# Kernel optimization log

Hardware: AMD Instinct MI355X
Metric: run time of the kernel (lower is better)

Reference implementation:

```python
import jax, jax.numpy as jnp
import numpy as np

IN_DIM = 128
OUT_DIM = 128
N_NEIGH = 32
BATCH = 8192


def setup_inputs() -> dict:
    key = jax.random.key(0)
    k1, k2, k3, k4, k5 = jax.random.split(key, 5)
    ai_sq = jax.random.normal(k1, (BATCH, IN_DIM), dtype=jnp.float32)
    ai_sn = jax.random.normal(k2, (N_NEIGH, BATCH, IN_DIM), dtype=jnp.float32)
    # nn.Linear params (weight [out,in], bias [out]) and attention vector u [2*out]
    W_w = jax.random.normal(k3, (OUT_DIM, IN_DIM), dtype=jnp.float32) / np.sqrt(IN_DIM)
    W_b = jax.random.normal(k4, (OUT_DIM,), dtype=jnp.float32) * 0.01
    u = jax.random.normal(k5, (2 * OUT_DIM,), dtype=jnp.float32)
    return {"ai_sq": ai_sq, "ai_sn": ai_sn, "W_w": W_w, "W_b": W_b, "u": u}


def reference(ai_sq, ai_sn, W_w, W_b, u):
    out_dim = W_w.shape[0]
    # shared linear projection W
    sq_proj = ai_sq @ W_w.T + W_b                      # [B, D]
    sn_proj = jnp.einsum('nbi,oi->nbo', ai_sn, W_w) + W_b  # [N, B, D]
    # u . concat(sq_proj, sn_proj) == u1.sq_proj + u2.sn_proj
    u1, u2 = u[:out_dim], u[out_dim:]
    mult = (sq_proj @ u1)[None, :] + jnp.einsum('nbd,d->nb', sn_proj, u2)  # [N, B]
    beta = jnp.exp(jax.nn.leaky_relu(mult, negative_slope=0.01))           # [N, B]
    return beta / jnp.sum(beta, axis=0)                # softmax-like normalize over neighbors
```

## Files before the change

kernel.cpp:

```cpp
#include <hip/hip_runtime.h>
#include <math.h>

#define IN_DIM   128
#define OUT_DIM  128
#define N_NEIGH  32
#define BATCH    8192
#define B_TILE   8

__global__ __launch_bounds__(1024) void prep_kernel(const float* __restrict__ W_w,
                                                    const float* __restrict__ W_b,
                                                    const float* __restrict__ u,
                                                    float* __restrict__ ws) {
    const int tid = threadIdx.x;
    const int i = tid & 127;
    const int g = tid >> 7;

    float a1 = 0.f, a2 = 0.f;
    #pragma unroll
    for (int oo = 0; oo < 16; ++oo) {
        int o = g * 16 + oo;
        float w = W_w[o * IN_DIM + i];
        a1 += w * u[o];
        a2 += w * u[OUT_DIM + o];
    }

    __shared__ float r1[8][128];
    __shared__ float r2[8][128];
    r1[g][i] = a1;
    r2[g][i] = a2;

    __shared__ float red[128];
    if (tid < 128) red[tid] = W_b[tid] * (u[tid] + u[OUT_DIM + tid]);
    __syncthreads();

    if (g == 0) {
        float s1 = 0.f, s2 = 0.f;
        #pragma unroll
        for (int gg = 0; gg < 8; ++gg) { s1 += r1[gg][i]; s2 += r2[gg][i]; }
        ws[i] = s1;
        ws[IN_DIM + i] = s2;
    }
    __syncthreads();
    if (tid == 0) {
        float s = 0.f;
        for (int k = 0; k < 128; ++k) s += red[k];
        ws[2 * IN_DIM] = s;
    }
}

__global__ __launch_bounds__(256) void gat_kernel(const float* __restrict__ ai_sq,
                                                  const float* __restrict__ ai_sn,
                                                  const float* __restrict__ ws,
                                                  float* __restrict__ out) {
    const int b0   = blockIdx.x * B_TILE;
    const int tid  = threadIdx.x;
    const int wave = tid >> 6;
    const int lane = tid & 63;
    const int c    = lane & 31;
    const int hb   = lane >> 5;

    __shared__ float t[33][B_TILE + 1];

    const float4* v1 = (const float4*)ws;
    const float4* v2 = (const float4*)(ws + IN_DIM);
    const float   cc = ws[2 * IN_DIM];
    const float4  v1c = v1[c];
    const float4  v2c = v2[c];

    for (int r = wave; r < 33; r += 4) {
        const float* base = (r < 32)
            ? (ai_sn + ((size_t)r * BATCH + b0) * IN_DIM)
            : (ai_sq + (size_t)b0 * IN_DIM);
        const float4 vv = (r < 32) ? v2c : v1c;
        #pragma unroll
        for (int k = 0; k < B_TILE / 2; ++k) {
            const int bl = k * 2 + hb;
            float4 x = ((const float4*)(base + (size_t)bl * IN_DIM))[c];
            float p = x.x * vv.x + x.y * vv.y + x.z * vv.z + x.w * vv.w;
            #pragma unroll
            for (int m = 16; m > 0; m >>= 1) p += __shfl_xor(p, m);
            if (c == 0) t[r][bl] = p;
        }
    }
    __syncthreads();

    const int n  = tid & 31;
    const int bl = tid >> 5;
    float mult = t[n][bl] + t[32][bl] + cc;
    float l = mult > 0.f ? mult : 0.01f * mult;
    float mx = l;
    #pragma unroll
    for (int m = 16; m > 0; m >>= 1) mx = fmaxf(mx, __shfl_xor(mx, m));
    float e = expf(l - mx);
    float s = e;
    #pragma unroll
    for (int m = 16; m > 0; m >>= 1) s += __shfl_xor(s, m);
    float res = e / s;
    __syncthreads();
    t[n][bl] = res;
    __syncthreads();

    const int nn = tid >> 3;
    const int bb = tid & 7;
    out[(size_t)nn * BATCH + b0 + bb] = t[nn][bb];
}

extern "C" void kernel_launch(void* const* d_in, const int* in_sizes, int n_in,
                              void* d_out, int out_size, void* d_ws, size_t ws_size,
                              hipStream_t stream) {
    const float* ai_sq = (const float*)d_in[0];
    const float* ai_sn = (const float*)d_in[1];
    const float* W_w   = (const float*)d_in[2];
    const float* W_b   = (const float*)d_in[3];
    const float* u     = (const float*)d_in[4];
    float* out = (float*)d_out;
    float* ws  = (float*)d_ws;

    prep_kernel<<<1, 1024, 0, stream>>>(W_w, W_b, u, ws);
    gat_kernel<<<BATCH / B_TILE, 256, 0, stream>>>(ai_sq, ai_sn, ws, out);
}
```

Baseline: 203.3 us.

## Fuse weight-vector prep into main kernel and software-pipeline neighbor loads

Removes the separate single-block prep kernel: each block recomputes W^T·u1, W^T·u2 and the bias constant into shared memory, then runs the attention computation. The main loop now has each wave handle one batch row across all 32 neighbors, with register double-buffering of four float4 loads per step and a segmented shuffle reduction that reduces four dot products together. The batch tile doubles to 16 with 512 threads. This removes one launch and the serial dependency on prep, and raises memory-level parallelism. The cost is redundant reads of the 64KB weight matrix in every block (512 blocks), served mostly from cache.

After: 203.4 us. No clear change (+0.1%).

```diff
diff --git a/kernel.cpp b/kernel.cpp
--- a/kernel.cpp
+++ b/kernel.cpp
@@ -5,104 +5,127 @@
 #define OUT_DIM  128
 #define N_NEIGH  32
 #define BATCH    8192
-#define B_TILE   8
+#define B_TILE   16
+#define THREADS  512
 
-__global__ __launch_bounds__(1024) void prep_kernel(const float* __restrict__ W_w,
-                                                    const float* __restrict__ W_b,
-                                                    const float* __restrict__ u,
-                                                    float* __restrict__ ws) {
+__global__ __launch_bounds__(THREADS) void gat_fused(const float* __restrict__ ai_sq,
+                                                     const float* __restrict__ ai_sn,
+                                                     const float* __restrict__ W_w,
+                                                     const float* __restrict__ W_b,
+                                                     const float* __restrict__ u,
+                                                     float* __restrict__ out) {
     const int tid = threadIdx.x;
-    const int i = tid & 127;
-    const int g = tid >> 7;
+    const int b0  = blockIdx.x * B_TILE;
 
-    float a1 = 0.f, a2 = 0.f;
-    #pragma unroll
-    for (int oo = 0; oo < 16; ++oo) {
-        int o = g * 16 + oo;
-        float w = W_w[o * IN_DIM + i];
-        a1 += w * u[o];
-        a2 += w * u[OUT_DIM + o];
+    __shared__ __align__(16) float v1s[IN_DIM];
+    __shared__ __align__(16) float v2s[IN_DIM];
+    __shared__ float r1s[4][IN_DIM];
+    __shared__ float r2s[4][IN_DIM];
+    __shared__ float ccs;
+
+    {
+        const int i = tid & 127;
+        const int g = tid >> 7;
+        float a1 = 0.f, a2 = 0.f;
+        #pragma unroll 8
+        for (int oo = 0; oo < 32; ++oo) {
+            const int o = g * 32 + oo;
+            const float w = W_w[o * IN_DIM + i];
+            a1 = fmaf(w, u[o], a1);
+            a2 = fmaf(w, u[OUT_DIM + o], a2);
+        }
+        r1s[g][i] = a1;
+        r2s[g][i] = a2;
+        if (tid < 64) {
+            float s = W_b[tid]      * (u[tid]      + u[OUT_DIM + tid])
+                    + W_b[tid + 64] * (u[tid + 64] + u[OUT_DIM + tid + 64]);
+            #pragma unroll
+            for (int m = 32; m > 0; m >>= 1) s += __shfl_xor(s, m);
+            if (tid == 0) ccs = s;
+        }
+        __syncthreads();
+        if (tid < 128) {
+            v1s[tid] = r1s[0][tid] + r1s[1][tid] + r1s[2][tid] + r1s[3][tid];
+            v2s[tid] = r2s[0][tid] + r2s[1][tid] + r2s[2][tid] + r2s[3][tid];
+        }
+        __syncthreads();
     }
 
-    __shared__ float r1[8][128];
-    __shared__ float r2[8][128];
-    r1[g][i] = a1;
-    r2[g][i] = a2;
-
-    __shared__ float red[128];
-    if (tid < 128) red[tid] = W_b[tid] * (u[tid] + u[OUT_DIM + tid]);
-    __syncthreads();
-
-    if (g == 0) {
-        float s1 = 0.f, s2 = 0.f;
-        #pragma unroll
-        for (int gg = 0; gg < 8; ++gg) { s1 += r1[gg][i]; s2 += r2[gg][i]; }
-        ws[i] = s1;
-        ws[IN_DIM + i] = s2;
-    }
-    __syncthreads();
-    if (tid == 0) {
-        float s = 0.f;
-        for (int k = 0; k < 128; ++k) s += red[k];
-        ws[2 * IN_DIM] = s;
-    }
-}
-
-__global__ __launch_bounds__(256) void gat_kernel(const float* __restrict__ ai_sq,
-                                                  const float* __restrict__ ai_sn,
-                                                  const float* __restrict__ ws,
-                                                  float* __restrict__ out) {
-    const int b0   = blockIdx.x * B_TILE;
-    const int tid  = threadIdx.x;
-    const int wave = tid >> 6;
     const int lane = tid & 63;
+    const int w    = tid >> 6;
     const int c    = lane & 31;
     const int hb   = lane >> 5;
+    const int bl   = 2 * w + hb;
+    const float4 v1c = ((const float4*)v1s)[c];
+    const float4 v2c = ((const float4*)v2s)[c];
+    const float  cc  = ccs;
 
-    __shared__ float t[33][B_TILE + 1];
+    __shared__ float t[N_NEIGH + 1][B_TILE + 1];
 
-    const float4* v1 = (const float4*)ws;
-    const float4* v2 = (const float4*)(ws + IN_DIM);
-    const float   cc = ws[2 * IN_DIM];
-    const float4  v1c = v1[c];
-    const float4  v2c = v2[c];
+    const size_t RS = (size_t)BATCH * (IN_DIM / 4);
+    const float4* p   = (const float4*)ai_sn + (size_t)(b0 + bl) * (IN_DIM / 4) + c;
+    const float4* psq = (const float4*)ai_sq + (size_t)(b0 + bl) * (IN_DIM / 4) + c;
 
-    for (int r = wave; r < 33; r += 4) {
-        const float* base = (r < 32)
-            ? (ai_sn + ((size_t)r * BATCH + b0) * IN_DIM)
-            : (ai_sq + (size_t)b0 * IN_DIM);
-        const float4 vv = (r < 32) ? v2c : v1c;
+    float4 q0 = p[0], q1 = p[RS], q2 = p[2 * RS], q3 = p[3 * RS];
+    #pragma unroll
+    for (int g = 0; g < 8; ++g) {
+        float4 n0, n1, n2, n3;
+        if (g < 7) {
+            const float4* pn = p + (size_t)(4 * g + 4) * RS;
+            n0 = pn[0]; n1 = pn[RS]; n2 = pn[2 * RS]; n3 = pn[3 * RS];
+        } else {
+            n0 = psq[0]; n1 = n0; n2 = n0; n3 = n0;
+        }
+        float d0 = fmaf(q0.x, v2c.x, fmaf(q0.y, v2c.y, fmaf(q0.z, v2c.z, q0.w * v2c.w)));
+        float d1 = fmaf(q1.x, v2c.x, fmaf(q1.y, v2c.y, fmaf(q1.z, v2c.z, q1.w * v2c.w)));
+        float d2 = fmaf(q2.x, v2c.x, fmaf(q2.y, v2c.y, fmaf(q2.z, v2c.z, q2.w * v2c.w)));
+        float d3 = fmaf(q3.x, v2c.x, fmaf(q3.y, v2c.y, fmaf(q3.z, v2c.z, q3.w * v2c.w)));
+
+        d0 += __shfl_xor(d0, 16); d1 += __shfl_xor(d1, 16);
+        d2 += __shfl_xor(d2, 16); d3 += __shfl_xor(d3, 16);
+        float e01 = (lane & 16) ? d1 : d0;
+        float e23 = (lane & 16) ? d3 : d2;
+        e01 += __shfl_xor(e01, 8);
+        e23 += __shfl_xor(e23, 8);
+        float z = (lane & 8) ? e23 : e01;
+        z += __shfl_xor(z, 4); z += __shfl_xor(z, 2); z += __shfl_xor(z, 1);
+        if ((lane & 7) == 0) {
+            const int rr = 4 * g + ((lane >> 3) & 1) * 2 + ((lane >> 4) & 1);
+            t[rr][bl] = z;
+        }
+        q0 = n0; q1 = n1; q2 = n2; q3 = n3;
+    }
+    {
+        float d = fmaf(q0.x, v1c.x, fmaf(q0.y, v1c.y, fmaf(q0.z, v1c.z, q0.w * v1c.w)));
         #pragma unroll
-        for (int k = 0; k < B_TILE / 2; ++k) {
-            const int bl = k * 2 + hb;
-            float4 x = ((const float4*)(base + (size_t)bl * IN_DIM))[c];
-            float p = x.x * vv.x + x.y * vv.y + x.z * vv.z + x.w * vv.w;
-            #pragma unroll
-            for (int m = 16; m > 0; m >>= 1) p += __shfl_xor(p, m);
-            if (c == 0) t[r][bl] = p;
-        }
+        for (int m = 16; m > 0; m >>= 1) d += __shfl_xor(d, m);
+        if (c == 0) t[N_NEIGH][bl] = d;
     }
     __syncthreads();
 
-    const int n  = tid & 31;
-    const int bl = tid >> 5;
-    float mult = t[n][bl] + t[32][bl] + cc;
-    float l = mult > 0.f ? mult : 0.01f * mult;
-    float mx = l;
-    #pragma unroll
-    for (int m = 16; m > 0; m >>= 1) mx = fmaxf(mx, __shfl_xor(mx, m));
-    float e = expf(l - mx);
-    float s = e;
-    #pragma unroll
-    for (int m = 16; m > 0; m >>= 1) s += __shfl_xor(s, m);
-    float res = e / s;
-    __syncthreads();
-    t[n][bl] = res;
+    {
+        const int n   = tid & 31;
+        const int blb = tid >> 5;
+        float mult = t[n][blb] + t[N_NEIGH][blb] + cc;
+        float l = mult > 0.f ? mult : 0.01f * mult;
+        float mx = l;
+        #pragma unroll
+        for (int m = 16; m > 0; m >>= 1) mx = fmaxf(mx, __shfl_xor(mx, m));
+        float e = expf(l - mx);
+        float s = e;
+        #pragma unroll
+        for (int m = 16; m > 0; m >>= 1) s += __shfl_xor(s, m);
+        float res = e / s;
+        __syncthreads();
+        t[n][blb] = res;
+    }
     __syncthreads();
 
-    const int nn = tid >> 3;
-    const int bb = tid & 7;
-    out[(size_t)nn * BATCH + b0 + bb] = t[nn][bb];
+    {
+        const int nn = tid >> 4;
+        const int bb = tid & 15;
+        out[(size_t)nn * BATCH + b0 + bb] = t[nn][bb];
+    }
 }
 
 extern "C" void kernel_launch(void* const* d_in, const int* in_sizes, int n_in,
@@ -114,8 +137,6 @@
     const float* W_b   = (const float*)d_in[3];
     const float* u     = (const float*)d_in[4];
     float* out = (float*)d_out;
-    float* ws  = (float*)d_ws;
 
-    prep_kernel<<<1, 1024, 0, stream>>>(W_w, W_b, u, ws);
-    gat_kernel<<<BATCH / B_TILE, 256, 0, stream>>>(ai_sq, ai_sn, ws, out);
+    gat_fused<<<BATCH / B_TILE, THREADS, 0, stream>>>(ai_sq, ai_sn, W_w, W_b, u, out);
 }
```
